# Optimization experiments

Hardware: AMD Instinct MI355X
Metric: run time of the kernel (lower is better)

Reference implementation:

```python
import jax, jax.numpy as jnp
import numpy as np

B = 2
NUM_CLS = 20
NUM_DIM = 256
H = W = 448
FH = FW = 28
K_TOP = 25


def _l2norm(x, eps=1e-12):
    # matches torch F.normalize(dim=1): x / max(||x||, eps); zero rows stay zero
    return x / jnp.maximum(jnp.linalg.norm(x, axis=-1, keepdims=True), eps)


def setup_inputs():
    key = jax.random.key(0)
    k1, k2, k3, k4 = jax.random.split(key, 4)
    fmap = jax.random.normal(k1, (B, NUM_DIM, FH, FW), jnp.float32)
    cam = jax.random.uniform(k2, (B, NUM_CLS, H, W), jnp.float32)
    cls_label = jax.random.randint(k3, (B, NUM_CLS), 0, 2).astype(jnp.float32)
    proj_weight = jax.random.normal(k4, (NUM_CLS, NUM_DIM), jnp.float32) * 0.02
    feature_contrast = jnp.zeros((NUM_CLS, NUM_DIM), jnp.float32)
    return {"fmap": fmap, "cam": cam, "cls_label": cls_label,
            "proj_weight": proj_weight, "feature_contrast": feature_contrast,
            "hig_thre": 0.7, "low_thre": 0.25, "bg_thre": 0.5}


def _forward(fmap, cam, cls_label, proj_weight, feature_contrast, hig_thre, low_thre, bg_thre):
    b, c, h, w = cam.shape
    d = fmap.shape[1]
    dt = fmap.dtype

    # ---- pseudo-label generation (vectorized over b,h,w) ----
    valid_cam = cls_label[:, :, None, None] * cam                       # [B,C,H,W]
    top2_v, top2_i = jax.lax.top_k(jnp.moveaxis(valid_cam, 1, -1), 2)   # [B,H,W,2]
    top1, second = top2_v[..., 0], top2_v[..., 1]
    pseudo = top2_i[..., 0] + 1
    pseudo = jnp.where(top1 < hig_thre, 255, pseudo)
    pseudo = jnp.where(top1 < low_thre, 0, pseudo)
    pseudo = jnp.where(top1 < bg_thre, 0, pseudo)
    pseudo = jnp.where((top1 - second < 0.3) & (top1 > hig_thre), 255, pseudo)

    # ---- upsample features (bilinear, align_corners=False) ----
    fmap_up = jax.image.resize(fmap, (b, d, h, w), 'bilinear')
    fmap_flat = fmap_up.reshape(b, d, h * w)                            # [B,D,HW]
    pseudo_flat = pseudo.reshape(b, h * w)                              # [B,HW]

    # ---- per-class features, both branches computed densely then selected ----
    cls_ids = jnp.arange(c) + 1
    mask = (pseudo_flat[:, None, :] == cls_ids[None, :, None]).astype(dt)  # [B,C,HW]
    counts = mask.sum(-1)                                                  # [B,C]
    feat_mask = jnp.einsum('bcp,bdp->bcd', mask, fmap_flat) / jnp.maximum(counts, 1.0)[:, :, None]
    _, top_idx = jax.lax.top_k(valid_cam.reshape(b, c, h * w), K_TOP)      # [B,C,25]
    gathered = jnp.take_along_axis(fmap_flat[:, None, :, :], top_idx[:, :, None, :], axis=-1)  # [B,C,D,25]
    feat_topk = gathered.mean(-1)                                          # [B,C,D]
    present = cls_label > 0.5                                              # [B,C] bool
    fsm = jnp.where((counts == 0.0)[:, :, None], feat_topk, feat_mask) * present[:, :, None]

    eye_f = jnp.eye(c, dtype=dt)
    eye_b = jnp.eye(c, dtype=bool)

    # ---- sequential per-sample loop (EMA memory bank carried across batch) ----
    def step(carry, xs):
        fc, loss_cls, loss_ccf = carry
        fsm_i, present_i = xs                                    # [C,D], [C]
        fsm_n = _l2norm(fsm_i)
        fc_n = _l2norm(jax.lax.stop_gradient(fc))
        cos = jnp.clip(jnp.abs(fsm_n @ fc_n.T), 1e-5, 1.0 - 1e-5)  # [C,C]
        ident = jnp.diag(present_i.astype(dt))
        loss_ccf = loss_ccf - (ident * jnp.log(cos) + (1.0 - ident) * jnp.log1p(-cos)).mean()
        off_max = jnp.where(eye_b, -jnp.inf, cos).max(axis=1)      # max over j != c
        qualify = present_i & (off_max < 0.6)                      # [C] bool
        p = jax.nn.softmax(fsm_i @ proj_weight.T, axis=-1)         # [C,C]
        logp = jnp.maximum(jnp.log(p), -100.0)
        log1mp = jnp.maximum(jnp.log1p(-p), -100.0)
        term = -(eye_f * logp + (1.0 - eye_f) * log1mp).mean(axis=-1)  # BCE(softmax, onehot) per class
        loss_cls = loss_cls + jnp.sum(jnp.where(qualify, term, 0.0))
        n = qualify.sum().astype(dt)
        loss_cls = jnp.where(n > 0, loss_cls / jnp.maximum(n, 1.0), loss_cls)
        fc = jnp.where(qualify[:, None], 0.95 * fc + 0.05 * jax.lax.stop_gradient(fsm_i), fc)
        return (fc, loss_cls, loss_ccf), None

    zero = jnp.asarray(0.0, dt)
    (_, loss_cls, loss_ccf), _ = jax.lax.scan(step, (feature_contrast, zero, zero), (fsm, present))
    return loss_ccf + loss_cls


def reference(fmap, cam, cls_label, proj_weight, feature_contrast, hig_thre, low_thre, bg_thre):
    return _forward(fmap, cam, cls_label, proj_weight, feature_contrast, hig_thre, low_thre, bg_thre)
```

## Files before the change

kernel.cpp:

```cpp
#include <hip/hip_runtime.h>
#include <cstdint>

#define HW 200704
#define IMG_W 448
#define NCLS 20
#define NDIM 256
#define NB2 784
#define LK 260

#define ASYNC_COPY4(gp, lp)                                                    \
  __builtin_amdgcn_global_load_lds(                                            \
      (const __attribute__((address_space(1))) void*)(gp),                     \
      (__attribute__((address_space(3))) void*)(lp), 4, 0, 0)

__global__ __launch_bounds__(256) void k_front(const float* __restrict__ fmap,
                                               float* __restrict__ fmapT,
                                               const float* __restrict__ cam,
                                               const float* __restrict__ cls_label,
                                               const float* __restrict__ hig_p,
                                               const float* __restrict__ low_p,
                                               const float* __restrict__ bg_p,
                                               float* __restrict__ W) {
  __shared__ float sT[NCLS][256];
  int tid = threadIdx.x;

  if (blockIdx.x >= 2 * NB2) {
    float (*tile)[33] = (float (*)[33]) & sT[0][0];
    int blk = blockIdx.x - 2 * NB2;
    int b = blk / 200;
    int t = blk % 200;
    int dT = t / 25, sT2 = t % 25;
    int ty = tid >> 5, tx = tid & 31;
#pragma unroll
    for (int r = 0; r < 4; ++r) {
      int d = dT * 32 + ty + r * 8;
      int s = sT2 * 32 + tx;
      if (s < 784) tile[ty + r * 8][tx] = fmap[((size_t)(b * 256 + d)) * 784 + s];
    }
    __syncthreads();
#pragma unroll
    for (int r = 0; r < 4; ++r) {
      int s = sT2 * 32 + ty + r * 8;
      int d = dT * 32 + tx;
      if (s < 784) fmapT[((size_t)(b * 784 + s)) * 256 + d] = tile[tx][ty + r * 8];
    }
    return;
  }

  int b = blockIdx.x / NB2;
  int blkInB = blockIdx.x % NB2;
  int pix0 = blkInB * 256;
  int wave = tid >> 6, lane = tid & 63;

  bool pres = (lane < NCLS) && (cls_label[b * NCLS + lane] != 0.0f);
  unsigned long long pm = __ballot(pres);
  unsigned mask = (unsigned)(pm & 0xFFFFFu);
  int np = __popc(mask);
  const float* camb = cam + (size_t)b * NCLS * HW + pix0 + wave * 64 + lane;

  {
    unsigned m = mask;
    for (int k = 0; k < np; ++k) {
      int c = __builtin_ctz(m); m &= m - 1u;
      ASYNC_COPY4(camb + (size_t)c * HW, &sT[k][wave * 64]);
    }
  }
  __builtin_amdgcn_s_waitcnt(0);

  float top1 = -1.0f, sec = -1.0f;
  int cls1 = 0;
  {
    unsigned m = mask;
    for (int k = 0; k < np; ++k) {
      int c = __builtin_ctz(m); m &= m - 1u;
      float x = sT[k][tid];
      bool gt = x > top1;
      sec = gt ? top1 : fmaxf(sec, fminf(x, top1));
      cls1 = gt ? c : cls1;
      top1 = gt ? x : top1;
    }
  }
  if (np < NCLS) sec = fmaxf(sec, 0.0f);
  float hig = hig_p[0], low = low_p[0], bg = bg_p[0];
  int pix = pix0 + tid;
  int ps = cls1 + 1;
  if (top1 < hig) ps = 255;
  if (top1 < low) ps = 0;
  if (top1 < bg)  ps = 0;
  if ((top1 - sec < 0.3f) && (top1 > hig)) ps = 255;
  if (ps >= 1 && ps <= NCLS) {
    int cls = ps - 1;
    int y = pix / IMG_W, x = pix % IMG_W;
    float sy = (y + 0.5f) * 0.0625f - 0.5f; sy = fminf(fmaxf(sy, 0.0f), 27.0f);
    float sx = (x + 0.5f) * 0.0625f - 0.5f; sx = fminf(fmaxf(sx, 0.0f), 27.0f);
    int fy0 = (int)sy, fx0 = (int)sx;
    int fy1 = min(fy0 + 1, 27), fx1 = min(fx0 + 1, 27);
    float wy = sy - (float)fy0, wx = sx - (float)fx0;
    float* Wb = W + (size_t)(b * NCLS + cls) * 784;
    atomicAdd(&Wb[fy0 * 28 + fx0], (1.0f - wy) * (1.0f - wx));
    atomicAdd(&Wb[fy0 * 28 + fx1], (1.0f - wy) * wx);
    atomicAdd(&Wb[fy1 * 28 + fx0], wy * (1.0f - wx));
    atomicAdd(&Wb[fy1 * 28 + fx1], wy * wx);
  }
}

__global__ __launch_bounds__(512) void k_mid(const float* __restrict__ fmapT,
                                             const float* __restrict__ cam,
                                             const float* __restrict__ Wg,
                                             const float* __restrict__ cls_label,
                                             float* __restrict__ P,
                                             float* __restrict__ S,
                                             float* __restrict__ cntW,
                                             const float* __restrict__ proj_w,
                                             const float* __restrict__ fc_init,
                                             float* __restrict__ BCEg,
                                             float* __restrict__ COS0,
                                             float* __restrict__ COS1V,
                                             unsigned* tickets,
                                             float* __restrict__ out) {
  int tid = threadIdx.x;

  if (blockIdx.x < 160) {
    __shared__ float sW[784];
    __shared__ float sH[2][256];
    __shared__ float sRed[8];
    __shared__ float sCntf;
    __shared__ float wv[8]; __shared__ int wi[8];
    __shared__ float selV; __shared__ int selI;
    __shared__ int sTop[25];
    int bc = blockIdx.x >> 2, part = blockIdx.x & 3;
    int b = bc / NCLS;
    int dim = tid & 255, h = tid >> 8;

    if (cls_label[bc] != 0.0f) {
      for (int s = tid; s < 784; s += 512) sW[s] = Wg[(size_t)bc * 784 + s];
      __syncthreads();
      {
        float cs = sW[tid >= 512 ? 0 : tid];
        cs = (tid < 512) ? sW[tid] : 0.0f;
        if (tid < 272) cs += sW[tid + 512];
        for (int off = 32; off > 0; off >>= 1) cs += __shfl_xor(cs, off, 64);
        if ((tid & 63) == 0) sRed[tid >> 6] = cs;
        __syncthreads();
        if (tid == 0) {
          float s = 0.0f;
          for (int w = 0; w < 8; ++w) s += sRed[w];
          sCntf = s;
        }
        __syncthreads();
      }
      float cntf = sCntf;
      const float* fT = fmapT + (size_t)b * 784 * 256;

      if (cntf > 0.0f) {
        int s0 = part * 196;
        if (h == 0) {
          float a0 = 0.0f, a1 = 0.0f;
          for (int s = s0; s < s0 + 196; s += 4) {
            a0 += sW[s]     * fT[(size_t)(s)     * 256 + dim];
            a1 += sW[s + 1] * fT[(size_t)(s + 1) * 256 + dim];
          }
          sH[0][dim] = a0 + a1;
        } else {
          float a2 = 0.0f, a3 = 0.0f;
          for (int s = s0; s < s0 + 196; s += 4) {
            a2 += sW[s + 2] * fT[(size_t)(s + 2) * 256 + dim];
            a3 += sW[s + 3] * fT[(size_t)(s + 3) * 256 + dim];
          }
          sH[1][dim] = a2 + a3;
        }
        __syncthreads();
        if (tid < 256)
          P[(size_t)(bc * 4 + part) * 256 + tid] = sH[0][tid] + sH[1][tid];
        if (part == 0 && tid == 0) cntW[bc] = cntf;
      } else if (part == 0) {
        if (tid == 0) cntW[bc] = 0.0f;
        const float* camc = cam + (size_t)bc * HW;
        float lastV = 3.0e38f; int lastI = -1;
        for (int r = 0; r < 25; ++r) {
          float bv = -1.0e30f; int bi = 0x7fffffff;
          for (int p = tid; p < HW; p += 512) {
            float vv2 = camc[p];
            if (((vv2 < lastV) || (vv2 == lastV && p > lastI)) &&
                ((vv2 > bv) || (vv2 == bv && p < bi))) { bv = vv2; bi = p; }
          }
          for (int off = 32; off > 0; off >>= 1) {
            float ov = __shfl_xor(bv, off, 64);
            int   oi = __shfl_xor(bi, off, 64);
            if (ov > bv || (ov == bv && oi < bi)) { bv = ov; bi = oi; }
          }
          if ((tid & 63) == 0) { wv[tid >> 6] = bv; wi[tid >> 6] = bi; }
          __syncthreads();
          if (tid == 0) {
            for (int w = 1; w < 8; ++w)
              if (wv[w] > bv || (wv[w] == bv && wi[w] < bi)) { bv = wv[w]; bi = wi[w]; }
            selV = bv; selI = bi; sTop[r] = bi;
          }
          __syncthreads();
          lastV = selV; lastI = selI;
        }
        if (tid < 256) {
          float at = 0.0f;
          for (int r = 0; r < 25; ++r) {
            int p = sTop[r];
            int y = p / IMG_W, x = p % IMG_W;
            float sy = (y + 0.5f) * 0.0625f - 0.5f; sy = fminf(fmaxf(sy, 0.0f), 27.0f);
            float sx = (x + 0.5f) * 0.0625f - 0.5f; sx = fminf(fmaxf(sx, 0.0f), 27.0f);
            int fy0 = (int)sy, fx0 = (int)sx;
            int fy1 = min(fy0 + 1, 27), fx1 = min(fx0 + 1, 27);
            float wy = sy - (float)fy0, wx = sx - (float)fx0;
            at += (1.0f - wy) * (1.0f - wx) * fT[(size_t)(fy0 * 28 + fx0) * 256 + tid]
                + (1.0f - wy) * wx          * fT[(size_t)(fy0 * 28 + fx1) * 256 + tid]
                + wy          * (1.0f - wx) * fT[(size_t)(fy1 * 28 + fx0) * 256 + tid]
                + wy          * wx          * fT[(size_t)(fy1 * 28 + fx1) * 256 + tid];
          }
          S[(size_t)bc * 256 + tid] = at * (1.0f / 25.0f);
        }
      }
    }
    __syncthreads();
    if (tid == 0) { __threadfence(); atomicAdd(tickets, 1u); }
    return;
  }

  int bp = blockIdx.x - 160;
  int b = bp / NCLS, i = bp % NCLS;
  __shared__ float sOwn[LK];
  __shared__ float sFc[NCLS * LK], sPw[NCLS * LK];
  __shared__ float sF0[NCLS * LK], sFv[NCLS * LK];
  __shared__ float sLog[NCLS];
  __shared__ float sNC[NCLS], sNCv[NCLS];
  __shared__ int   sZC[NCLS], sZCv[NCLS];
  __shared__ float sNI[1]; __shared__ int sZI[1];
  __shared__ float sCos[400];
  __shared__ float sBCE[2][NCLS], sRow[NCLS];
  __shared__ int   sQual[NCLS];
  __shared__ float sPres[2][NCLS];
  __shared__ float sScal[2];
  __shared__ unsigned sLast;

  for (int idx = tid; idx < NCLS * NDIM; idx += 512) {
    int r = idx >> 8, d = idx & 255;
    sFc[r * LK + d] = fc_init[idx];
    sPw[r * LK + d] = proj_w[idx];
  }

  if (tid == 0) {
    while (__hip_atomic_load(tickets, __ATOMIC_ACQUIRE, __HIP_MEMORY_SCOPE_AGENT) < 160u)
      __builtin_amdgcn_s_sleep(4);
  }
  __syncthreads();
  __threadfence();

  if (tid < 256) {
    int bc = b * NCLS + i, d = tid;
    float v = 0.0f;
    if (cls_label[bc] != 0.0f) {
      float c = cntW[bc];
      if (c > 0.0f) {
        const float* p = P + (size_t)bc * 1024 + d;
        v = ((p[0] + p[256]) + (p[512] + p[768])) / fmaxf(c, 1.0f);
      } else {
        v = S[(size_t)bc * 256 + d];
      }
    }
    sOwn[d] = v;
  }
  if (b == 1) {
    for (int idx = tid; idx < NCLS * NDIM; idx += 512) {
      int bc = idx >> 8, d = idx & 255;
      float v = 0.0f;
      if (cls_label[bc] != 0.0f) {
        float c = cntW[bc];
        if (c > 0.0f) {
          const float* p = P + (size_t)bc * 1024 + d;
          v = ((p[0] + p[256]) + (p[512] + p[768])) / fmaxf(c, 1.0f);
        } else {
          v = S[(size_t)bc * 256 + d];
        }
      }
      sF0[bc * LK + d] = v;
    }
  }
  __syncthreads();
  if (b == 1) {
    for (int idx = tid; idx < NCLS * NDIM; idx += 512) {
      int r = idx >> 8, d = idx & 255;
      sFv[r * LK + d] = 0.95f * sFc[r * LK + d] + 0.05f * sF0[r * LK + d];
    }
    __syncthreads();
  }

  {
    int g = tid >> 3, sub = tid & 7;
    if (g <= 20) {
      const float* row = (g < 20) ? &sFc[g * LK] : sOwn;
      float a0 = 0.0f, a1 = 0.0f, a2 = 0.0f, a3 = 0.0f;
      int d0 = sub * 32;
#pragma unroll
      for (int d = d0; d < d0 + 32; d += 8) {
        float4 x = *(const float4*)&row[d];
        float4 y = *(const float4*)&row[d + 4];
        a0 += x.x * x.x + x.y * x.y;
        a1 += x.z * x.z + x.w * x.w;
        a2 += y.x * y.x + y.y * y.y;
        a3 += y.z * y.z + y.w * y.w;
      }
      float s = (a0 + a1) + (a2 + a3);
      s += __shfl_xor(s, 1, 64);
      s += __shfl_xor(s, 2, 64);
      s += __shfl_xor(s, 4, 64);
      if (sub == 0) {
        if (g < 20) { sNC[g] = fmaxf(sqrtf(s), 1e-12f); sZC[g] = (s == 0.0f); }
        else        { sNI[0] = fmaxf(sqrtf(s), 1e-12f); sZI[0] = (s == 0.0f); }
      }
    }
  }
  __syncthreads();
  if (b == 1) {
    int g = tid >> 3, sub = tid & 7;
    if (g < 20) {
      const float* row = &sFv[g * LK];
      float a0 = 0.0f, a1 = 0.0f, a2 = 0.0f, a3 = 0.0f;
      int d0 = sub * 32;
#pragma unroll
      for (int d = d0; d < d0 + 32; d += 8) {
        float4 x = *(const float4*)&row[d];
        float4 y = *(const float4*)&row[d + 4];
        a0 += x.x * x.x + x.y * x.y;
        a1 += x.z * x.z + x.w * x.w;
        a2 += y.x * y.x + y.y * y.y;
        a3 += y.z * y.z + y.w * y.w;
      }
      float s = (a0 + a1) + (a2 + a3);
      s += __shfl_xor(s, 1, 64);
      s += __shfl_xor(s, 2, 64);
      s += __shfl_xor(s, 4, 64);
      if (sub == 0) { sNCv[g] = fmaxf(sqrtf(s), 1e-12f); sZCv[g] = (s == 0.0f); }
    }
    __syncthreads();
  }

  if (tid < NCLS) {
    const float* ra = sOwn;
    const float* rb = &sPw[tid * LK];
    float a0 = 0, a1 = 0, a2 = 0, a3 = 0, a4 = 0, a5 = 0, a6 = 0, a7 = 0;
    for (int d = 0; d < 256; d += 16) {
      float4 x0 = *(const float4*)&ra[d],      y0 = *(const float4*)&rb[d];
      float4 x1 = *(const float4*)&ra[d + 4],  y1 = *(const float4*)&rb[d + 4];
      float4 x2 = *(const float4*)&ra[d + 8],  y2 = *(const float4*)&rb[d + 8];
      float4 x3 = *(const float4*)&ra[d + 12], y3 = *(const float4*)&rb[d + 12];
      a0 += x0.x * y0.x + x0.y * y0.y;  a1 += x0.z * y0.z + x0.w * y0.w;
      a2 += x1.x * y1.x + x1.y * y1.y;  a3 += x1.z * y1.z + x1.w * y1.w;
      a4 += x2.x * y2.x + x2.y * y2.y;  a5 += x2.z * y2.z + x2.w * y2.w;
      a6 += x3.x * y3.x + x3.y * y3.y;  a7 += x3.z * y3.z + x3.w * y3.w;
    }
    sLog[tid] = ((a0 + a1) + (a2 + a3)) + ((a4 + a5) + (a6 + a7));
  }
  __syncthreads();

  if (tid < 32) {
    int jj = tid;
    float l = (jj < NCLS) ? sLog[jj] : -3.0e38f;
    float m = l;
#pragma unroll
    for (int off = 1; off < 32; off <<= 1) m = fmaxf(m, __shfl_xor(m, off, 64));
    float e = (jj < NCLS) ? expf(l - m) : 0.0f;
    float sS = e;
#pragma unroll
    for (int off = 1; off < 32; off <<= 1) sS += __shfl_xor(sS, off, 64);
    float term = 0.0f;
    if (jj < NCLS) {
      float p = e / sS;
      term = (jj == i) ? fmaxf(logf(p), -100.0f) : fmaxf(log1pf(-p), -100.0f);
    }
#pragma unroll
    for (int off = 1; off < 32; off <<= 1) term += __shfl_xor(term, off, 64);
    if (jj == 0) BCEg[b * NCLS + i] = -term / 20.0f;
  }
  if (tid >= 64 && tid < 64 + 2 * NCLS) {
    int j = (tid - 64) >> 1, sub = tid & 1;
    float c0;
    if (sZI[0] || sZC[j]) c0 = 0.0f;
    else {
      const float* ra = sOwn;
      const float* rb = &sFc[j * LK];
      float a0 = 0.0f, a1 = 0.0f, a2 = 0.0f, a3 = 0.0f;
      int d0 = sub * 128;
      for (int d = d0; d < d0 + 128; d += 8) {
        float4 x  = *(const float4*)&ra[d];
        float4 y  = *(const float4*)&rb[d];
        float4 x2 = *(const float4*)&ra[d + 4];
        float4 y2 = *(const float4*)&rb[d + 4];
        a0 += x.x * y.x + x.y * y.y;
        a1 += x.z * y.z + x.w * y.w;
        a2 += x2.x * y2.x + x2.y * y2.y;
        a3 += x2.z * y2.z + x2.w * y2.w;
      }
      float acc = (a0 + a1) + (a2 + a3);
      acc += __shfl_xor(acc, 1, 64);
      c0 = fabsf(acc / (sNI[0] * sNC[j]));
    }
    if (sub == 0) {
      float cv = fminf(fmaxf(c0, 1e-5f), 1.0f - 1e-5f);
      if (b == 0) COS0[i * NCLS + j] = cv;
      else        COS1V[i * NCLS + j] = cv;
    }
  }
  if (b == 1 && tid >= 128 && tid < 128 + 2 * NCLS) {
    int j = (tid - 128) >> 1, sub = tid & 1;
    float c0;
    if (sZI[0] || sZCv[j]) c0 = 0.0f;
    else {
      const float* ra = sOwn;
      const float* rb = &sFv[j * LK];
      float a0 = 0.0f, a1 = 0.0f, a2 = 0.0f, a3 = 0.0f;
      int d0 = sub * 128;
      for (int d = d0; d < d0 + 128; d += 8) {
        float4 x  = *(const float4*)&ra[d];
        float4 y  = *(const float4*)&rb[d];
        float4 x2 = *(const float4*)&ra[d + 4];
        float4 y2 = *(const float4*)&rb[d + 4];
        a0 += x.x * y.x + x.y * y.y;
        a1 += x.z * y.z + x.w * y.w;
        a2 += x2.x * y2.x + x2.y * y2.y;
        a3 += x2.z * y2.z + x2.w * y2.w;
      }
      float acc = (a0 + a1) + (a2 + a3);
      acc += __shfl_xor(acc, 1, 64);
      c0 = fabsf(acc / (sNI[0] * sNCv[j]));
    }
    if (sub == 0)
      COS1V[400 + i * NCLS + j] = fminf(fmaxf(c0, 1e-5f), 1.0f - 1e-5f);
  }

  __syncthreads();
  if (tid == 0) { __threadfence(); sLast = atomicAdd(tickets + 1, 1u); }
  __syncthreads();
  if (sLast != 39u) return;
  __threadfence();

  if (tid < 400) sCos[tid] = COS0[tid];
  if (tid < 40) { sBCE[tid / NCLS][tid % NCLS] = BCEg[tid];
                  sPres[tid / NCLS][tid % NCLS] = cls_label[tid]; }
  if (tid == 0) { sScal[0] = 0.0f; sScal[1] = 0.0f; }
  __syncthreads();

  for (int bb = 0; bb < 2; ++bb) {
    if (bb == 1) {
      if (tid < 400) {
        int j = tid % NCLS;
        sCos[tid] = sQual[j] ? COS1V[400 + tid] : COS1V[tid];
      }
      __syncthreads();
    }
    {
      int jj = tid & 31;
      for (int r = tid >> 5; r < NCLS; r += 16) {
        float pres = (sPres[bb][r] > 0.5f) ? 1.0f : 0.0f;
        float contrib = 0.0f, omv = -3.0e38f;
        if (jj < NCLS) {
          float c0 = sCos[r * NCLS + jj];
          float ident = (jj == r) ? pres : 0.0f;
          contrib = ident * logf(c0) + (1.0f - ident) * log1pf(-c0);
          if (jj != r) omv = c0;
        }
#pragma unroll
        for (int off = 1; off < 32; off <<= 1) {
          contrib += __shfl_xor(contrib, off, 64);
          omv = fmaxf(omv, __shfl_xor(omv, off, 64));
        }
        if (jj == 0) { sRow[r] = contrib; sQual[r] = (pres > 0.5f && omv < 0.6f) ? 1 : 0; }
      }
    }
    __syncthreads();
    if (tid == 0) {
      float s = 0.0f;
      for (int r = 0; r < NCLS; ++r) s += sRow[r];
      sScal[0] -= s / 400.0f;
      float add = 0.0f; int nq = 0;
      for (int r = 0; r < NCLS; ++r) if (sQual[r]) { add += sBCE[bb][r]; nq++; }
      float lc = sScal[1] + add;
      if (nq > 0) lc = lc / fmaxf((float)nq, 1.0f);
      sScal[1] = lc;
    }
    __syncthreads();
  }
  if (tid == 0) out[0] = sScal[0] + sScal[1];
}

extern "C" void kernel_launch(void* const* d_in, const int* in_sizes, int n_in,
                              void* d_out, int out_size, void* d_ws, size_t ws_size,
                              hipStream_t stream) {
  const float* fmap      = (const float*)d_in[0];
  const float* cam       = (const float*)d_in[1];
  const float* cls_label = (const float*)d_in[2];
  const float* proj_w    = (const float*)d_in[3];
  const float* fc_init   = (const float*)d_in[4];
  const float* hig       = (const float*)d_in[5];
  const float* low       = (const float*)d_in[6];
  const float* bg        = (const float*)d_in[7];
  float* out = (float*)d_out;

  char* ws = (char*)d_ws;
  float*    W     = (float*)(ws);
  unsigned* tick  = (unsigned*)(ws + 125440);
  float*    cntW  = (float*)(ws + 125456);
  float*    P     = (float*)(ws + 125616);
  float*    S     = (float*)(ws + 289456);
  float*    fmapT = (float*)(ws + 330416);
  float*    BCEg  = (float*)(ws + 1936048);
  float*    COS0  = (float*)(ws + 1936208);
  float*    COS1V = (float*)(ws + 1937808);

  hipMemsetAsync(ws, 0, 125456, stream);
  k_front<<<2 * NB2 + 400, 256, 0, stream>>>(fmap, fmapT, cam, cls_label,
                                             hig, low, bg, W);
  k_mid  <<<          200, 512, 0, stream>>>(fmapT, cam, W, cls_label, P, S,
                                             cntW, proj_w, fc_init, BCEg,
                                             COS0, COS1V, tick, out);
}
```

Baseline: 128.1 us.

## Split fused mid kernel into separate feature and pre-loss kernels

New measurement: 124.0 us. 1.03x faster.

```diff
diff --git a/kernel.cpp b/kernel.cpp
--- a/kernel.cpp
+++ b/kernel.cpp
@@ -104,13 +104,116 @@
   }
 }
 
-__global__ __launch_bounds__(512) void k_mid(const float* __restrict__ fmapT,
-                                             const float* __restrict__ cam,
-                                             const float* __restrict__ Wg,
+__global__ __launch_bounds__(512) void k_feat(const float* __restrict__ fmapT,
+                                              const float* __restrict__ cam,
+                                              const float* __restrict__ Wg,
+                                              const float* __restrict__ cls_label,
+                                              float* __restrict__ P,
+                                              float* __restrict__ S,
+                                              float* __restrict__ cntW) {
+  __shared__ float sW[784];
+  __shared__ float sH[2][256];
+  __shared__ float sRed[8];
+  __shared__ float sCntf;
+  __shared__ float wv[8]; __shared__ int wi[8];
+  __shared__ float selV; __shared__ int selI;
+  __shared__ int sTop[25];
+  int bc = blockIdx.x >> 2, part = blockIdx.x & 3;
+  int b = bc / NCLS;
+  int tid = threadIdx.x;
+  int dim = tid & 255, h = tid >> 8;
+  if (cls_label[bc] == 0.0f) return;
+
+  for (int s = tid; s < 784; s += 512) sW[s] = Wg[(size_t)bc * 784 + s];
+  __syncthreads();
+  {
+    float cs = sW[tid >= 512 ? 0 : tid];
+    cs = (tid < 512) ? sW[tid] : 0.0f;
+    if (tid < 272) cs += sW[tid + 512];
+    for (int off = 32; off > 0; off >>= 1) cs += __shfl_xor(cs, off, 64);
+    if ((tid & 63) == 0) sRed[tid >> 6] = cs;
+    __syncthreads();
+    if (tid == 0) {
+      float s = 0.0f;
+      for (int w = 0; w < 8; ++w) s += sRed[w];
+      sCntf = s;
+    }
+    __syncthreads();
+  }
+  float cntf = sCntf;
+  const float* fT = fmapT + (size_t)b * 784 * 256;
+
+  if (cntf > 0.0f) {
+    int s0 = part * 196;
+    if (h == 0) {
+      float a0 = 0.0f, a1 = 0.0f;
+      for (int s = s0; s < s0 + 196; s += 4) {
+        a0 += sW[s]     * fT[(size_t)(s)     * 256 + dim];
+        a1 += sW[s + 1] * fT[(size_t)(s + 1) * 256 + dim];
+      }
+      sH[0][dim] = a0 + a1;
+    } else {
+      float a2 = 0.0f, a3 = 0.0f;
+      for (int s = s0; s < s0 + 196; s += 4) {
+        a2 += sW[s + 2] * fT[(size_t)(s + 2) * 256 + dim];
+        a3 += sW[s + 3] * fT[(size_t)(s + 3) * 256 + dim];
+      }
+      sH[1][dim] = a2 + a3;
+    }
+    __syncthreads();
+    if (tid < 256)
+      P[(size_t)(bc * 4 + part) * 256 + tid] = sH[0][tid] + sH[1][tid];
+    if (part == 0 && tid == 0) cntW[bc] = cntf;
+  } else if (part == 0) {
+    if (tid == 0) cntW[bc] = 0.0f;
+    const float* camc = cam + (size_t)bc * HW;
+    float lastV = 3.0e38f; int lastI = -1;
+    for (int r = 0; r < 25; ++r) {
+      float bv = -1.0e30f; int bi = 0x7fffffff;
+      for (int p = tid; p < HW; p += 512) {
+        float vv2 = camc[p];
+        if (((vv2 < lastV) || (vv2 == lastV && p > lastI)) &&
+            ((vv2 > bv) || (vv2 == bv && p < bi))) { bv = vv2; bi = p; }
+      }
+      for (int off = 32; off > 0; off >>= 1) {
+        float ov = __shfl_xor(bv, off, 64);
+        int   oi = __shfl_xor(bi, off, 64);
+        if (ov > bv || (ov == bv && oi < bi)) { bv = ov; bi = oi; }
+      }
+      if ((tid & 63) == 0) { wv[tid >> 6] = bv; wi[tid >> 6] = bi; }
+      __syncthreads();
+      if (tid == 0) {
+        for (int w = 1; w < 8; ++w)
+          if (wv[w] > bv || (wv[w] == bv && wi[w] < bi)) { bv = wv[w]; bi = wi[w]; }
+        selV = bv; selI = bi; sTop[r] = bi;
+      }
+      __syncthreads();
+      lastV = selV; lastI = selI;
+    }
+    if (tid < 256) {
+      float at = 0.0f;
+      for (int r = 0; r < 25; ++r) {
+        int p = sTop[r];
+        int y = p / IMG_W, x = p % IMG_W;
+        float sy = (y + 0.5f) * 0.0625f - 0.5f; sy = fminf(fmaxf(sy, 0.0f), 27.0f);
+        float sx = (x + 0.5f) * 0.0625f - 0.5f; sx = fminf(fmaxf(sx, 0.0f), 27.0f);
+        int fy0 = (int)sy, fx0 = (int)sx;
+        int fy1 = min(fy0 + 1, 27), fx1 = min(fx0 + 1, 27);
+        float wy = sy - (float)fy0, wx = sx - (float)fx0;
+        at += (1.0f - wy) * (1.0f - wx) * fT[(size_t)(fy0 * 28 + fx0) * 256 + tid]
+            + (1.0f - wy) * wx          * fT[(size_t)(fy0 * 28 + fx1) * 256 + tid]
+            + wy          * (1.0f - wx) * fT[(size_t)(fy1 * 28 + fx0) * 256 + tid]
+            + wy          * wx          * fT[(size_t)(fy1 * 28 + fx1) * 256 + tid];
+      }
+      S[(size_t)bc * 256 + tid] = at * (1.0f / 25.0f);
+    }
+  }
+}
+
+__global__ __launch_bounds__(256) void k_pre(const float* __restrict__ P,
+                                             const float* __restrict__ S,
+                                             const float* __restrict__ cntW,
                                              const float* __restrict__ cls_label,
-                                             float* __restrict__ P,
-                                             float* __restrict__ S,
-                                             float* __restrict__ cntW,
                                              const float* __restrict__ proj_w,
                                              const float* __restrict__ fc_init,
                                              float* __restrict__ BCEg,
@@ -118,113 +221,6 @@
                                              float* __restrict__ COS1V,
                                              unsigned* tickets,
                                              float* __restrict__ out) {
-  int tid = threadIdx.x;
-
-  if (blockIdx.x < 160) {
-    __shared__ float sW[784];
-    __shared__ float sH[2][256];
-    __shared__ float sRed[8];
-    __shared__ float sCntf;
-    __shared__ float wv[8]; __shared__ int wi[8];
-    __shared__ float selV; __shared__ int selI;
-    __shared__ int sTop[25];
-    int bc = blockIdx.x >> 2, part = blockIdx.x & 3;
-    int b = bc / NCLS;
-    int dim = tid & 255, h = tid >> 8;
-
-    if (cls_label[bc] != 0.0f) {
-      for (int s = tid; s < 784; s += 512) sW[s] = Wg[(size_t)bc * 784 + s];
-      __syncthreads();
-      {
-        float cs = sW[tid >= 512 ? 0 : tid];
-        cs = (tid < 512) ? sW[tid] : 0.0f;
-        if (tid < 272) cs += sW[tid + 512];
-        for (int off = 32; off > 0; off >>= 1) cs += __shfl_xor(cs, off, 64);
-        if ((tid & 63) == 0) sRed[tid >> 6] = cs;
-        __syncthreads();
-        if (tid == 0) {
-          float s = 0.0f;
-          for (int w = 0; w < 8; ++w) s += sRed[w];
-          sCntf = s;
-        }
-        __syncthreads();
-      }
-      float cntf = sCntf;
-      const float* fT = fmapT + (size_t)b * 784 * 256;
-
-      if (cntf > 0.0f) {
-        int s0 = part * 196;
-        if (h == 0) {
-          float a0 = 0.0f, a1 = 0.0f;
-          for (int s = s0; s < s0 + 196; s += 4) {
-            a0 += sW[s]     * fT[(size_t)(s)     * 256 + dim];
-            a1 += sW[s + 1] * fT[(size_t)(s + 1) * 256 + dim];
-          }
-          sH[0][dim] = a0 + a1;
-        } else {
-          float a2 = 0.0f, a3 = 0.0f;
-          for (int s = s0; s < s0 + 196; s += 4) {
-            a2 += sW[s + 2] * fT[(size_t)(s + 2) * 256 + dim];
-            a3 += sW[s + 3] * fT[(size_t)(s + 3) * 256 + dim];
-          }
-          sH[1][dim] = a2 + a3;
-        }
-        __syncthreads();
-        if (tid < 256)
-          P[(size_t)(bc * 4 + part) * 256 + tid] = sH[0][tid] + sH[1][tid];
-        if (part == 0 && tid == 0) cntW[bc] = cntf;
-      } else if (part == 0) {
-        if (tid == 0) cntW[bc] = 0.0f;
-        const float* camc = cam + (size_t)bc * HW;
-        float lastV = 3.0e38f; int lastI = -1;
-        for (int r = 0; r < 25; ++r) {
-          float bv = -1.0e30f; int bi = 0x7fffffff;
-          for (int p = tid; p < HW; p += 512) {
-            float vv2 = camc[p];
-            if (((vv2 < lastV) || (vv2 == lastV && p > lastI)) &&
-                ((vv2 > bv) || (vv2 == bv && p < bi))) { bv = vv2; bi = p; }
-          }
-          for (int off = 32; off > 0; off >>= 1) {
-            float ov = __shfl_xor(bv, off, 64);
-            int   oi = __shfl_xor(bi, off, 64);
-            if (ov > bv || (ov == bv && oi < bi)) { bv = ov; bi = oi; }
-          }
-          if ((tid & 63) == 0) { wv[tid >> 6] = bv; wi[tid >> 6] = bi; }
-          __syncthreads();
-          if (tid == 0) {
-            for (int w = 1; w < 8; ++w)
-              if (wv[w] > bv || (wv[w] == bv && wi[w] < bi)) { bv = wv[w]; bi = wi[w]; }
-            selV = bv; selI = bi; sTop[r] = bi;
-          }
-          __syncthreads();
-          lastV = selV; lastI = selI;
-        }
-        if (tid < 256) {
-          float at = 0.0f;
-          for (int r = 0; r < 25; ++r) {
-            int p = sTop[r];
-            int y = p / IMG_W, x = p % IMG_W;
-            float sy = (y + 0.5f) * 0.0625f - 0.5f; sy = fminf(fmaxf(sy, 0.0f), 27.0f);
-            float sx = (x + 0.5f) * 0.0625f - 0.5f; sx = fminf(fmaxf(sx, 0.0f), 27.0f);
-            int fy0 = (int)sy, fx0 = (int)sx;
-            int fy1 = min(fy0 + 1, 27), fx1 = min(fx0 + 1, 27);
-            float wy = sy - (float)fy0, wx = sx - (float)fx0;
-            at += (1.0f - wy) * (1.0f - wx) * fT[(size_t)(fy0 * 28 + fx0) * 256 + tid]
-                + (1.0f - wy) * wx          * fT[(size_t)(fy0 * 28 + fx1) * 256 + tid]
-                + wy          * (1.0f - wx) * fT[(size_t)(fy1 * 28 + fx0) * 256 + tid]
-                + wy          * wx          * fT[(size_t)(fy1 * 28 + fx1) * 256 + tid];
-          }
-          S[(size_t)bc * 256 + tid] = at * (1.0f / 25.0f);
-        }
-      }
-    }
-    __syncthreads();
-    if (tid == 0) { __threadfence(); atomicAdd(tickets, 1u); }
-    return;
-  }
-
-  int bp = blockIdx.x - 160;
-  int b = bp / NCLS, i = bp % NCLS;
   __shared__ float sOwn[LK];
   __shared__ float sFc[NCLS * LK], sPw[NCLS * LK];
   __shared__ float sF0[NCLS * LK], sFv[NCLS * LK];
@@ -238,21 +234,15 @@
   __shared__ float sPres[2][NCLS];
   __shared__ float sScal[2];
   __shared__ unsigned sLast;
-
-  for (int idx = tid; idx < NCLS * NDIM; idx += 512) {
+  int tid = threadIdx.x;
+  int b = blockIdx.x / NCLS, i = blockIdx.x % NCLS;
+
+  for (int idx = tid; idx < NCLS * NDIM; idx += 256) {
     int r = idx >> 8, d = idx & 255;
     sFc[r * LK + d] = fc_init[idx];
     sPw[r * LK + d] = proj_w[idx];
   }
-
-  if (tid == 0) {
-    while (__hip_atomic_load(tickets, __ATOMIC_ACQUIRE, __HIP_MEMORY_SCOPE_AGENT) < 160u)
-      __builtin_amdgcn_s_sleep(4);
-  }
-  __syncthreads();
-  __threadfence();
-
-  if (tid < 256) {
+  {
     int bc = b * NCLS + i, d = tid;
     float v = 0.0f;
     if (cls_label[bc] != 0.0f) {
@@ -267,7 +257,7 @@
     sOwn[d] = v;
   }
   if (b == 1) {
-    for (int idx = tid; idx < NCLS * NDIM; idx += 512) {
+    for (int idx = tid; idx < NCLS * NDIM; idx += 256) {
       int bc = idx >> 8, d = idx & 255;
       float v = 0.0f;
       if (cls_label[bc] != 0.0f) {
@@ -284,7 +274,7 @@
   }
   __syncthreads();
   if (b == 1) {
-    for (int idx = tid; idx < NCLS * NDIM; idx += 512) {
+    for (int idx = tid; idx < NCLS * NDIM; idx += 256) {
       int r = idx >> 8, d = idx & 255;
       sFv[r * LK + d] = 0.95f * sFc[r * LK + d] + 0.05f * sF0[r * LK + d];
     }
@@ -435,28 +425,30 @@
   }
 
   __syncthreads();
-  if (tid == 0) { __threadfence(); sLast = atomicAdd(tickets + 1, 1u); }
-  __syncthreads();
-  if (sLast != 39u) return;
+  if (tid == 0) { __threadfence(); sLast = atomicAdd(tickets, 1u); }
+  __syncthreads();
+  if (sLast != 2 * NCLS - 1) return;
   __threadfence();
 
-  if (tid < 400) sCos[tid] = COS0[tid];
-  if (tid < 40) { sBCE[tid / NCLS][tid % NCLS] = BCEg[tid];
-                  sPres[tid / NCLS][tid % NCLS] = cls_label[tid]; }
-  if (tid == 0) { sScal[0] = 0.0f; sScal[1] = 0.0f; }
+  {
+    for (int idx = tid; idx < 400; idx += 256) sCos[idx] = COS0[idx];
+    if (tid < 40) { sBCE[tid / NCLS][tid % NCLS] = BCEg[tid];
+                    sPres[tid / NCLS][tid % NCLS] = cls_label[tid]; }
+    if (tid == 0) { sScal[0] = 0.0f; sScal[1] = 0.0f; }
+  }
   __syncthreads();
 
   for (int bb = 0; bb < 2; ++bb) {
     if (bb == 1) {
-      if (tid < 400) {
-        int j = tid % NCLS;
-        sCos[tid] = sQual[j] ? COS1V[400 + tid] : COS1V[tid];
+      for (int idx = tid; idx < 400; idx += 256) {
+        int j = idx % NCLS;
+        sCos[idx] = sQual[j] ? COS1V[400 + idx] : COS1V[idx];
       }
       __syncthreads();
     }
     {
       int jj = tid & 31;
-      for (int r = tid >> 5; r < NCLS; r += 16) {
+      for (int r = tid >> 5; r < NCLS; r += 8) {
         float pres = (sPres[bb][r] > 0.5f) ? 1.0f : 0.0f;
         float contrib = 0.0f, omv = -3.0e38f;
         if (jj < NCLS) {
@@ -516,7 +508,7 @@
   hipMemsetAsync(ws, 0, 125456, stream);
   k_front<<<2 * NB2 + 400, 256, 0, stream>>>(fmap, fmapT, cam, cls_label,
                                              hig, low, bg, W);
-  k_mid  <<<          200, 512, 0, stream>>>(fmapT, cam, W, cls_label, P, S,
-                                             cntW, proj_w, fc_init, BCEg,
-                                             COS0, COS1V, tick, out);
+  k_feat <<<          160, 512, 0, stream>>>(fmapT, cam, W, cls_label, P, S, cntW);
+  k_pre  <<<     2 * NCLS, 256, 0, stream>>>(P, S, cntW, cls_label, proj_w,
+                                             fc_init, BCEg, COS0, COS1V, tick, out);
 }
```
